# Kernel optimization log

Hardware: AMD Instinct MI355X
Metric: run time of the kernel (lower is better)

Reference implementation:

```python
import jax, jax.numpy as jnp
import numpy as np


def _step(state):
    # state: [B, H, W] in {0.0, 1.0}
    p = jnp.pad(state, ((0, 0), (1, 1), (1, 1)))
    neighbors = (p[:, :-2, :-2] + p[:, :-2, 1:-1] + p[:, :-2, 2:]
                 + p[:, 1:-1, :-2] + p[:, 1:-1, 2:]
                 + p[:, 2:, :-2] + p[:, 2:, 1:-1] + p[:, 2:, 2:])
    alive = state > 0.5
    survives = alive & ((neighbors == 2.0) | (neighbors == 3.0))
    born = (~alive) & (neighbors == 3.0)
    return jnp.where(survives | born, jnp.ones_like(state), jnp.zeros_like(state))


def setup_inputs() -> dict:
    key = jax.random.key(0)
    k1, k2 = jax.random.split(key)
    B, H, W = 32, 1024, 1024
    # Binary occupancy grids in {0.0, 1.0} as the rule expects
    initial_state = (jax.random.uniform(k1, (B, H, W)) > 0.5).astype(jnp.float32)
    target = (jax.random.uniform(k2, (B, H, W)) > 0.5).astype(jnp.float32)
    return {"initial_state": initial_state, "target": target, "generations": 8}


def reference(initial_state, target, generations):
    state = initial_state
    for _ in range(generations):  # small fixed unroll, strict sequential dependency
        state = _step(state)
    error = state - target
    loss = jnp.mean(error * error)
    live_cells = state.sum()
    max_abs_error = jnp.abs(error).max()
    return loss, state, target, live_cells, max_abs_error
```

## Files before the change

### kernel.cpp

```cpp
#include <hip/hip_runtime.h>
#include <cstdint>

typedef unsigned long long u64;

#define BATCH   32
#define H       1024
#define W       1024
#define WPR     16
#define TR      64
#define HALO    8
#define BR      (TR + 2*HALO)
#define BRP     (BR + 2)
#define WP      (WPR + 2)
#define THREADS 512
#define NWAVES  (THREADS/64)
#define GENS    8
#define GRID    (BATCH * (H / TR))
#define NTOT    33554432ULL

__device__ __forceinline__ u64 shflxor64(u64 v, int m) {
    return (u64)__shfl_xor((long long)v, m, 64);
}

__global__ __launch_bounds__(THREADS)
void gol_fused(const float* __restrict__ in_state,
               const float* __restrict__ target,
               float* __restrict__ out,
               u64* __restrict__ counters)
{
    __shared__ u64 buf[2][BRP][WP];
    __shared__ unsigned int wsum[NWAVES];

    const int tile = blockIdx.x;
    const int tpb  = H / TR;
    const int b    = tile / tpb;
    const int r0   = (tile - b * tpb) * TR;

    const int tid  = threadIdx.x;
    const int wave = tid >> 6;
    const int lane = tid & 63;

    for (int i = tid; i < 2 * BRP * WP; i += THREADS)
        ((u64*)buf)[i] = 0ULL;
    __syncthreads();

    const size_t boff = (size_t)b * H * W;
    const float* inb  = in_state + boff;

    const int sub   = lane & 15;
    const int wsub  = lane >> 4;
    for (int br = wave; br < BR; br += NWAVES) {
        int gr = r0 - HALO + br;
        if (gr < 0 || gr >= H) continue;
        const float4* rowp4 = (const float4*)(inb + (size_t)gr * W);
        #pragma unroll
        for (int g = 0; g < 4; ++g) {
            float4 f = rowp4[g * 64 + lane];
            u64 nib = (u64)((f.x > 0.5f) | ((f.y > 0.5f) << 1) |
                            ((f.z > 0.5f) << 2) | ((f.w > 0.5f) << 3));
            u64 v = nib << (sub * 4);
            v |= shflxor64(v, 1);
            v |= shflxor64(v, 2);
            v |= shflxor64(v, 4);
            v |= shflxor64(v, 8);
            if (sub == 0)
                buf[0][br + 1][g * 4 + wsub + 1] = v;
        }
    }
    __syncthreads();

    int cur = 0;
    for (int step = 0; step < GENS; ++step) {
        for (int idx = tid; idx < BR * WPR; idx += THREADS) {
            int br = idx >> 4;
            int c  = (idx & 15) + 1;
            int r  = br + 1;
            int gr = r0 - HALO + br;

            u64 uL = buf[cur][r-1][c-1], uC = buf[cur][r-1][c], uR = buf[cur][r-1][c+1];
            u64 mL = buf[cur][r  ][c-1], mC = buf[cur][r  ][c], mR = buf[cur][r  ][c+1];
            u64 dL = buf[cur][r+1][c-1], dC = buf[cur][r+1][c], dR = buf[cur][r+1][c+1];

            u64 uw = (uC << 1) | (uL >> 63), ue = (uC >> 1) | (uR << 63);
            u64 mw = (mC << 1) | (mL >> 63), me = (mC >> 1) | (mR << 63);
            u64 dw = (dC << 1) | (dL >> 63), de = (dC >> 1) | (dR << 63);
            u64 o0 = uw ^ uC ^ ue, t0 = (uw & uC) | (ue & (uw ^ uC));
            u64 o1 = mw ^ mC ^ me, t1 = (mw & mC) | (me & (mw ^ mC));
            u64 o2 = dw ^ dC ^ de, t2 = (dw & dC) | (de & (dw ^ dC));

            u64 oa = o0 ^ o1 ^ o2;
            u64 oc = (o0 & o1) | (o2 & (o0 ^ o1));
            u64 ts = t0 ^ t1 ^ t2;
            u64 tc = (t0 & t1) | (t2 & (t0 ^ t1));
            u64 b1 = oc ^ ts;
            u64 cc = oc & ts;
            u64 b2 = cc ^ tc;
            u64 b3 = cc & tc;
            u64 eq3 = oa & b1 & ~(b2 | b3);
            u64 eq4 = (~oa) & (~b1) & b2 & (~b3);
            u64 nxtw = eq3 | (mC & eq4);

            buf[cur ^ 1][r][c] = (gr >= 0 && gr < H) ? nxtw : 0ULL;
        }
        __syncthreads();
        cur ^= 1;
    }

    float* o_state = out + 1;
    float* o_tgt   = out + 1 + NTOT;

    unsigned int mism = 0, live = 0;
    for (int lr = wave; lr < TR; lr += NWAVES) {
        int br = HALO + lr;
        int gr = r0 + lr;
        size_t rowbase = boff + (size_t)gr * W;
        const u64* wrow = &buf[cur][br + 1][1];
        const float* trow = target + rowbase;
        float* osrow = o_state + rowbase;
        float* otrow = o_tgt + rowbase;
        #pragma unroll
        for (int g = 0; g < 4; ++g) {
            int k = g * 64 + lane;
            if (k < 255) {
                int bitbase = 4 * k + 3;
                int w0 = bitbase >> 6;
                int sh = bitbase & 63;
                u64 lo = wrow[w0];
                u64 hi = wrow[w0 + 1];
                unsigned bits = (unsigned)(((lo >> sh) | (hi << (64 - sh))) & 0xFULL);
                float4 t = *(const float4*)(trow + bitbase);
                unsigned tb = (unsigned)((t.x > 0.5f) | ((t.y > 0.5f) << 1) |
                                         ((t.z > 0.5f) << 2) | ((t.w > 0.5f) << 3));
                mism += (unsigned)__popc(bits ^ tb);
                live += (unsigned)__popc(bits);
                float4 sv;
                sv.x = (float)(bits & 1u);
                sv.y = (float)((bits >> 1) & 1u);
                sv.z = (float)((bits >> 2) & 1u);
                sv.w = (float)((bits >> 3) & 1u);
                *(float4*)(osrow + bitbase) = sv;
                *(float4*)(otrow + bitbase) = t;
            } else {
                u64 wfirst = wrow[0];
                u64 wlast  = wrow[15];
                unsigned hb  = (unsigned)(wfirst & 7ULL);
                unsigned tbit = (unsigned)(wlast >> 63);
                float t0 = trow[0], t1 = trow[1], t2 = trow[2], t3 = trow[1023];
                unsigned htb = (unsigned)((t0 > 0.5f) | ((t1 > 0.5f) << 1) | ((t2 > 0.5f) << 2));
                unsigned ttb = (unsigned)(t3 > 0.5f);
                mism += (unsigned)__popc(hb ^ htb) + (tbit ^ ttb);
                live += (unsigned)__popc(hb) + tbit;
                osrow[0] = (float)(hb & 1u);
                osrow[1] = (float)((hb >> 1) & 1u);
                osrow[2] = (float)((hb >> 2) & 1u);
                osrow[1023] = (float)tbit;
                otrow[0] = t0; otrow[1] = t1; otrow[2] = t2; otrow[1023] = t3;
            }
        }
    }

    unsigned int comb = (mism << 16) | live;
    #pragma unroll
    for (int m = 1; m < 64; m <<= 1)
        comb += (unsigned int)__shfl_xor((int)comb, m, 64);
    if (lane == 0) wsum[wave] = comb;
    __syncthreads();

    if (tid == 0) {
        unsigned int bm = 0, bl = 0;
        #pragma unroll
        for (int i = 0; i < NWAVES; ++i) {
            bm += wsum[i] >> 16;
            bl += wsum[i] & 0xFFFFu;
        }
        atomicAdd(counters, ((u64)bm << 32) | (u64)bl);
    }
}

__global__ void gol_finalize(const u64* __restrict__ counters,
                             float* __restrict__ out)
{
    u64 c = *counters;
    unsigned int mism = (unsigned int)(c >> 32);
    unsigned int live = (unsigned int)(c & 0xFFFFFFFFULL);
    out[0]            = (float)((double)mism / (double)NTOT);
    out[1 + 2*NTOT]   = (float)live;
    out[2 + 2*NTOT]   = (mism > 0) ? 1.0f : 0.0f;
}

extern "C" void kernel_launch(void* const* d_in, const int* in_sizes, int n_in,
                              void* d_out, int out_size, void* d_ws, size_t ws_size,
                              hipStream_t stream) {
    (void)in_sizes; (void)n_in; (void)out_size; (void)ws_size;
    const float* in_state = (const float*)d_in[0];
    const float* target   = (const float*)d_in[1];
    float* out = (float*)d_out;
    u64* counters = (u64*)d_ws;

    hipMemsetAsync(d_ws, 0, sizeof(u64), stream);

    gol_fused<<<dim3(GRID), dim3(THREADS), 0, stream>>>(in_state, target, out, counters);
    gol_finalize<<<1, 1, 0, stream>>>(counters, out);
}
```

Baseline: 461.5 us.

## Shrink halo compute per generation, process row pairs, fold finalize into last block

Each generation now updates only the band of rows still needed for the final tile, which narrows by one row on each side per step, instead of the full haloed tile. Each thread computes two adjacent output rows so the horizontal partial sums of the shared middle rows are reused, cutting shared-memory loads and bit logic. The separate finalize kernel is replaced by a last-block ticket counter inside the main kernel, removing one launch. Rows outside the band keep stale values but are never read by later valid rows. The ticket path relies on fences and atomics for ordering.

Result: slower. 495.9 us (+7.4%).

```diff
diff --git a/kernel.cpp b/kernel.cpp
--- a/kernel.cpp
+++ b/kernel.cpp
@@ -20,6 +20,28 @@
 
 __device__ __forceinline__ u64 shflxor64(u64 v, int m) {
     return (u64)__shfl_xor((long long)v, m, 64);
+}
+
+__device__ __forceinline__ void hrow(u64 L, u64 C, u64 R, u64& o, u64& t) {
+    u64 wv = (C << 1) | (L >> 63);
+    u64 ev = (C >> 1) | (R << 63);
+    o = wv ^ C ^ ev;
+    t = (wv & C) | (ev & (wv ^ C));
+}
+
+__device__ __forceinline__ u64 life_next(u64 oA, u64 tA, u64 oB, u64 tB,
+                                         u64 oC, u64 tC, u64 mid) {
+    u64 oa = oA ^ oB ^ oC;
+    u64 oc = (oA & oB) | (oC & (oA ^ oB));
+    u64 ts = tA ^ tB ^ tC;
+    u64 tc = (tA & tB) | (tC & (tA ^ tB));
+    u64 b1 = oc ^ ts;
+    u64 cc = oc & ts;
+    u64 b2 = cc ^ tc;
+    u64 b3 = cc & tc;
+    u64 eq3 = oa & b1 & ~(b2 | b3);
+    u64 eq4 = (~oa) & (~b1) & b2 & (~b3);
+    return eq3 | (mid & eq4);
 }
 
 __global__ __launch_bounds__(THREADS)
@@ -71,36 +93,31 @@
 
     int cur = 0;
     for (int step = 0; step < GENS; ++step) {
-        for (int idx = tid; idx < BR * WPR; idx += THREADS) {
-            int br = idx >> 4;
-            int c  = (idx & 15) + 1;
-            int r  = br + 1;
-            int gr = r0 - HALO + br;
-
-            u64 uL = buf[cur][r-1][c-1], uC = buf[cur][r-1][c], uR = buf[cur][r-1][c+1];
-            u64 mL = buf[cur][r  ][c-1], mC = buf[cur][r  ][c], mR = buf[cur][r  ][c+1];
-            u64 dL = buf[cur][r+1][c-1], dC = buf[cur][r+1][c], dR = buf[cur][r+1][c+1];
-
-            u64 uw = (uC << 1) | (uL >> 63), ue = (uC >> 1) | (uR << 63);
-            u64 mw = (mC << 1) | (mL >> 63), me = (mC >> 1) | (mR << 63);
-            u64 dw = (dC << 1) | (dL >> 63), de = (dC >> 1) | (dR << 63);
-            u64 o0 = uw ^ uC ^ ue, t0 = (uw & uC) | (ue & (uw ^ uC));
-            u64 o1 = mw ^ mC ^ me, t1 = (mw & mC) | (me & (mw ^ mC));
-            u64 o2 = dw ^ dC ^ de, t2 = (dw & dC) | (de & (dw ^ dC));
-
-            u64 oa = o0 ^ o1 ^ o2;
-            u64 oc = (o0 & o1) | (o2 & (o0 ^ o1));
-            u64 ts = t0 ^ t1 ^ t2;
-            u64 tc = (t0 & t1) | (t2 & (t0 ^ t1));
-            u64 b1 = oc ^ ts;
-            u64 cc = oc & ts;
-            u64 b2 = cc ^ tc;
-            u64 b3 = cc & tc;
-            u64 eq3 = oa & b1 & ~(b2 | b3);
-            u64 eq4 = (~oa) & (~b1) & b2 & (~b3);
-            u64 nxtw = eq3 | (mC & eq4);
-
-            buf[cur ^ 1][r][c] = (gr >= 0 && gr < H) ? nxtw : 0ULL;
+        const int lo     = step + 1;
+        const int npairs = 39 - step;
+        const int items  = npairs * WPR;
+        for (int idx = tid; idx < items; idx += THREADS) {
+            int pr  = idx >> 4;
+            int c   = (idx & 15) + 1;
+            int br0 = lo + 2 * pr;
+            int r   = br0 + 1;
+
+            u64 o0, t0, o1, t1, o2, t2, o3, t3, mB, mC;
+            { u64 L = buf[cur][r-1][c-1], C = buf[cur][r-1][c], R = buf[cur][r-1][c+1];
+              hrow(L, C, R, o0, t0); }
+            { u64 L = buf[cur][r  ][c-1], C = buf[cur][r  ][c], R = buf[cur][r  ][c+1];
+              hrow(L, C, R, o1, t1); mB = C; }
+            { u64 L = buf[cur][r+1][c-1], C = buf[cur][r+1][c], R = buf[cur][r+1][c+1];
+              hrow(L, C, R, o2, t2); mC = C; }
+            { u64 L = buf[cur][r+2][c-1], C = buf[cur][r+2][c], R = buf[cur][r+2][c+1];
+              hrow(L, C, R, o3, t3); }
+
+            u64 n0 = life_next(o0, t0, o1, t1, o2, t2, mB);
+            u64 n1 = life_next(o1, t1, o2, t2, o3, t3, mC);
+
+            int gr0 = r0 - HALO + br0;
+            buf[cur ^ 1][r    ][c] = (gr0     >= 0 && gr0     < H) ? n0 : 0ULL;
+            buf[cur ^ 1][r + 1][c] = (gr0 + 1 >= 0 && gr0 + 1 < H) ? n1 : 0ULL;
         }
         __syncthreads();
         cur ^= 1;
@@ -173,19 +190,19 @@
             bm += wsum[i] >> 16;
             bl += wsum[i] & 0xFFFFu;
         }
-        atomicAdd(counters, ((u64)bm << 32) | (u64)bl);
-    }
-}
-
-__global__ void gol_finalize(const u64* __restrict__ counters,
-                             float* __restrict__ out)
-{
-    u64 c = *counters;
-    unsigned int mism = (unsigned int)(c >> 32);
-    unsigned int live = (unsigned int)(c & 0xFFFFFFFFULL);
-    out[0]            = (float)((double)mism / (double)NTOT);
-    out[1 + 2*NTOT]   = (float)live;
-    out[2 + 2*NTOT]   = (mism > 0) ? 1.0f : 0.0f;
+        atomicAdd(&counters[0], ((u64)bm << 32) | (u64)bl);
+        __threadfence();
+        u64 tk = atomicAdd(&counters[1], 1ULL);
+        if (tk == (u64)(GRID - 1)) {
+            __threadfence();
+            u64 c = atomicAdd(&counters[0], 0ULL);
+            unsigned int tmism = (unsigned int)(c >> 32);
+            unsigned int tlive = (unsigned int)(c & 0xFFFFFFFFULL);
+            out[0]            = (float)((double)tmism / (double)NTOT);
+            out[1 + 2*NTOT]   = (float)tlive;
+            out[2 + 2*NTOT]   = (tmism > 0) ? 1.0f : 0.0f;
+        }
+    }
 }
 
 extern "C" void kernel_launch(void* const* d_in, const int* in_sizes, int n_in,
@@ -197,8 +214,7 @@
     float* out = (float*)d_out;
     u64* counters = (u64*)d_ws;
 
-    hipMemsetAsync(d_ws, 0, sizeof(u64), stream);
+    hipMemsetAsync(d_ws, 0, 2 * sizeof(u64), stream);
 
     gol_fused<<<dim3(GRID), dim3(THREADS), 0, stream>>>(in_state, target, out, counters);
-    gol_finalize<<<1, 1, 0, stream>>>(counters, out);
-}
+}
```
